# Optimization experiments

Hardware: AMD Instinct MI355X
Metric: run time of the kernel (lower is better)

## Reference

```python
import jax, jax.numpy as jnp
import numpy as np

EPS = 1e-5
B, CIN, COUT, H, W = 32, 512, 512, 56, 56
K = 4            # kernel_num
A = 32           # attention_channel = max(int(512*0.0625), 16)


def setup_inputs() -> dict:
    key = jax.random.key(0)
    ks = jax.random.split(key, 16)
    s = lambda fan: 1.0 / np.sqrt(fan)
    return {
        "x": jax.random.normal(ks[0], (B, CIN, H, W), jnp.float32),
        # attention trunk: global-avgpool -> fc -> bn -> relu
        "fc_w": jax.random.normal(ks[1], (A, CIN), jnp.float32) * s(CIN),
        "abn_g": jnp.ones((A,), jnp.float32),
        "abn_b": jnp.zeros((A,), jnp.float32),
        "abn_m": jax.random.normal(ks[2], (A,), jnp.float32) * 0.1,
        "abn_v": jax.random.uniform(ks[3], (A,), jnp.float32, 0.5, 1.5),
        # channel / filter / kernel attention heads
        "ch_w": jax.random.normal(ks[4], (CIN, A), jnp.float32) * s(A),
        "ch_b": jnp.zeros((CIN,), jnp.float32),
        "fl_w": jax.random.normal(ks[5], (COUT, A), jnp.float32) * s(A),
        "fl_b": jnp.zeros((COUT,), jnp.float32),
        "kn_w": jax.random.normal(ks[6], (K, A), jnp.float32) * s(A),
        "kn_b": jnp.zeros((K,), jnp.float32),
        # base 1x1 conv weight bank [kernel_num, out, in] (1x1 spatial squeezed)
        "weight": jax.random.normal(ks[7], (K, COUT, CIN), jnp.float32) * s(CIN),
        # output BatchNorm2d (eval mode: running stats)
        "bn_g": jnp.ones((COUT,), jnp.float32),
        "bn_b": jnp.zeros((COUT,), jnp.float32),
        "bn_m": jax.random.normal(ks[8], (COUT,), jnp.float32) * 0.1,
        "bn_v": jax.random.uniform(ks[9], (COUT,), jnp.float32, 0.5, 1.5),
    }


def reference(x, fc_w, abn_g, abn_b, abn_m, abn_v,
              ch_w, ch_b, fl_w, fl_b, kn_w, kn_b,
              weight, bn_g, bn_b, bn_m, bn_v):
    # ---- omni-dimensional attention (kernel_size=1 => spatial attn skipped) ----
    pooled = jnp.mean(x, axis=(2, 3))                       # [B, Cin]
    h = pooled @ fc_w.T                                     # [B, A]
    h = (h - abn_m) * (abn_g / jnp.sqrt(abn_v + EPS)) + abn_b
    h = jax.nn.relu(h)
    ch_att = jax.nn.sigmoid(h @ ch_w.T + ch_b)              # [B, Cin]
    fl_att = jax.nn.sigmoid(h @ fl_w.T + fl_b)              # [B, Cout]
    kn_att = jax.nn.softmax(h @ kn_w.T + kn_b, axis=1)      # [B, K] (temperature=1)
    # ---- per-sample aggregated 1x1 kernel + grouped(batch) pointwise conv ----
    agg_w = jnp.einsum('bk,koc->boc', kn_att, weight)       # [B, Cout, Cin]
    xm = x * ch_att[:, :, None, None]                       # channel attention
    y = jnp.einsum('bchw,boc->bohw', xm, agg_w)             # batched 1x1 conv
    y = y * fl_att[:, :, None, None]                        # filter attention
    # ---- BatchNorm2d (inference) ----
    inv = bn_g / jnp.sqrt(bn_v + EPS)
    y = (y - bn_m[None, :, None, None]) * inv[None, :, None, None] + bn_b[None, :, None, None]
    return y
```

## Files before the change

### kernel.cpp

```cpp
#include <hip/hip_runtime.h>
#include <math.h>

#define BATCH 32
#define CIN   512
#define COUT  512
#define HW    3136
#define KNUM  4
#define ADIM  32
#define EPS   1e-5f

static constexpr size_t XT_OFF    = 0;
static constexpr size_t WF_OFF    = 102760448;
static constexpr size_t PART_OFF  = 119537664;
static constexpr size_t CH_OFF    = 122748928;
static constexpr size_t FLINV_OFF = 122814464;
static constexpr size_t KN_OFF    = 122880000;

typedef __attribute__((ext_vector_type(8))) short short8;
typedef __attribute__((ext_vector_type(4))) float float4v;

typedef const unsigned int __attribute__((address_space(1)))* gas_ptr;
typedef unsigned int __attribute__((address_space(3)))* lds_ptr;

__device__ __forceinline__ unsigned short f2bf(float f) {
  unsigned int u = __float_as_uint(f);
  u += 0x7FFFu + ((u >> 16) & 1u);
  return (unsigned short)(u >> 16);
}

__global__ __launch_bounds__(256) void transpose_pool(
    const float* __restrict__ x, unsigned short* __restrict__ xT,
    float* __restrict__ part) {
  __shared__ unsigned short T[64 * 68];
  const int pb    = blockIdx.x * 64;
  const int cbase = blockIdx.y * 256;
  const int b     = blockIdx.z;
  const int t  = threadIdx.x;
  const int mp = t & 15;
  const int mc = t >> 4;
  const int p0 = pb + mp * 4;
  const int pr = t >> 2, cp = t & 3;

  #pragma unroll
  for (int sub = 0; sub < 4; ++sub) {
    const int cb = cbase + sub * 64;
    const int c0 = cb + mc * 4;
    const float* xp = x + (size_t)(b * CIN + c0) * HW + p0;
    float a[4][4];
    #pragma unroll
    for (int r = 0; r < 4; ++r) {
      float4 v = *(const float4*)(xp + (size_t)r * HW);
      a[r][0] = v.x; a[r][1] = v.y; a[r][2] = v.z; a[r][3] = v.w;
      float s = v.x + v.y + v.z + v.w;
      #pragma unroll
      for (int off = 8; off > 0; off >>= 1) s += __shfl_down(s, off, 16);
      if (mp == 0)
        part[((size_t)b * 49 + blockIdx.x) * 512 + c0 + r] = s;
    }
    #pragma unroll
    for (int j = 0; j < 4; ++j) {
      ushort4 w;
      w.x = f2bf(a[0][j]); w.y = f2bf(a[1][j]);
      w.z = f2bf(a[2][j]); w.w = f2bf(a[3][j]);
      *(ushort4*)&T[(mp * 4 + j) * 68 + mc * 4] = w;
    }
    __syncthreads();
    const int base = pr * 68 + cp * 16;
    uint2 r0 = *(uint2*)&T[base + 0];
    uint2 r1 = *(uint2*)&T[base + 4];
    uint2 r2 = *(uint2*)&T[base + 8];
    uint2 r3 = *(uint2*)&T[base + 12];
    unsigned short* dst = xT + (size_t)(b * HW + pb + pr) * CIN + cb + cp * 16;
    *(uint4*)(dst)     = make_uint4(r0.x, r0.y, r1.x, r1.y);
    *(uint4*)(dst + 8) = make_uint4(r2.x, r2.y, r3.x, r3.y);
    __syncthreads();
  }
}

__global__ __launch_bounds__(256) void attn_all(
    const float* __restrict__ part, const float* __restrict__ fc_w,
    const float* __restrict__ abn_g, const float* __restrict__ abn_b,
    const float* __restrict__ abn_m, const float* __restrict__ abn_v,
    const float* __restrict__ kn_w, const float* __restrict__ kn_b,
    const float* __restrict__ ch_w, const float* __restrict__ ch_b,
    const float* __restrict__ fl_w, const float* __restrict__ fl_b,
    const float* __restrict__ bn_g, const float* __restrict__ bn_v,
    float* __restrict__ ch_out, float* __restrict__ flinv_out,
    float* __restrict__ kn_out) {
  __shared__ float pooledS[CIN];
  __shared__ float hs[ADIM];
  const int b = blockIdx.x, t = threadIdx.x;
  #pragma unroll
  for (int idx = t; idx < CIN; idx += 256) {
    float s = 0.f;
    for (int j = 0; j < 49; ++j) s += part[((size_t)b * 49 + j) * 512 + idx];
    pooledS[idx] = s;
  }
  __syncthreads();
  {
    const int a = t >> 3, pz = t & 7;
    const float* fr = fc_w + a * CIN + pz * 64;
    const float* pp = pooledS + pz * 64;
    float s = 0.f;
    #pragma unroll 8
    for (int c = 0; c < 64; ++c) s += pp[c] * fr[c];
    #pragma unroll
    for (int off = 4; off > 0; off >>= 1) s += __shfl_down(s, off, 8);
    if (pz == 0) {
      s *= (1.0f / (float)HW);
      float vv = (s - abn_m[a]) * (abn_g[a] * rsqrtf(abn_v[a] + EPS)) + abn_b[a];
      hs[a] = fmaxf(vv, 0.f);
    }
  }
  __syncthreads();
  if (t == 0) {
    float lg[KNUM]; float mx = -1e30f;
    for (int k = 0; k < KNUM; ++k) {
      float acc = kn_b[k];
      for (int aa = 0; aa < ADIM; ++aa) acc += hs[aa] * kn_w[k * ADIM + aa];
      lg[k] = acc; mx = fmaxf(mx, acc);
    }
    float ssum = 0.f;
    for (int k = 0; k < KNUM; ++k) { lg[k] = expf(lg[k] - mx); ssum += lg[k]; }
    for (int k = 0; k < KNUM; ++k) kn_out[b * KNUM + k] = lg[k] / ssum;
  }
  #pragma unroll
  for (int c = t; c < CIN; c += 256) {
    const float* wr = ch_w + c * ADIM;
    float acc = ch_b[c];
    #pragma unroll
    for (int aa = 0; aa < ADIM; ++aa) acc += hs[aa] * wr[aa];
    ch_out[b * CIN + c] = 1.f / (1.f + expf(-acc));
  }
  #pragma unroll
  for (int o = t; o < COUT; o += 256) {
    const float* wr = fl_w + o * ADIM;
    float acc = fl_b[o];
    #pragma unroll
    for (int aa = 0; aa < ADIM; ++aa) acc += hs[aa] * wr[aa];
    float sig = 1.f / (1.f + expf(-acc));
    flinv_out[b * COUT + o] = sig * (bn_g[o] * rsqrtf(bn_v[o] + EPS));
  }
}

__global__ __launch_bounds__(256) void build_wf(
    const float* __restrict__ weight, const float* __restrict__ kn,
    const float* __restrict__ ch, const float* __restrict__ flinv,
    unsigned short* __restrict__ Wf) {
  const int och = blockIdx.x, b = blockIdx.y, t = threadIdx.x;
  const int o0 = och * 16;
  const float k0 = kn[b * KNUM + 0], k1 = kn[b * KNUM + 1];
  const float k2 = kn[b * KNUM + 2], k3 = kn[b * KNUM + 3];
  #pragma unroll
  for (int i = 0; i < 8; ++i) {
    int cell = i * 1024 + t * 4;
    int ol = cell >> 9, c = cell & 511;
    int o = o0 + ol;
    float fi = flinv[b * COUT + o];
    const float* wp = weight + (size_t)o * CIN + c;
    float4 w0 = *(const float4*)(wp);
    float4 w1 = *(const float4*)(wp + 1 * CIN * COUT);
    float4 w2 = *(const float4*)(wp + 2 * CIN * COUT);
    float4 w3 = *(const float4*)(wp + 3 * CIN * COUT);
    float4 cv = *(const float4*)(ch + b * CIN + c);
    ushort4 r;
    r.x = f2bf((k0 * w0.x + k1 * w1.x + k2 * w2.x + k3 * w3.x) * cv.x * fi);
    r.y = f2bf((k0 * w0.y + k1 * w1.y + k2 * w2.y + k3 * w3.y) * cv.y * fi);
    r.z = f2bf((k0 * w0.z + k1 * w1.z + k2 * w2.z + k3 * w3.z) * cv.z * fi);
    r.w = f2bf((k0 * w0.w + k1 * w1.w + k2 * w2.w + k3 * w3.w) * cv.w * fi);
    *(ushort4*)(Wf + (size_t)(b * COUT + o) * CIN + c) = r;
  }
}

__global__ __launch_bounds__(256, 4) void gemm_kernel(
    const unsigned short* __restrict__ xT, const unsigned short* __restrict__ Wf,
    const float* __restrict__ bn_g, const float* __restrict__ bn_b,
    const float* __restrict__ bn_m, const float* __restrict__ bn_v,
    float* __restrict__ y) {
  __shared__ unsigned short lA[128 * 64];
  __shared__ unsigned short lB[128 * 64];
  const int ot = blockIdx.x, pt = blockIdx.y, b = blockIdx.z;
  const int o0 = ot * 128, p0 = pt * 128;
  const int t = threadIdx.x;
  const int wave = t >> 6, lane = t & 63;
  const int wm = wave & 1, wn = wave >> 1;

  const int srow = lane >> 3;
  const int sgrp = lane & 7;
  const int scol = ((sgrp ^ srow) * 8);

  const unsigned short* Ab = Wf + (size_t)b * COUT * CIN;
  const unsigned short* Bb = xT + (size_t)b * HW * CIN;
  const unsigned short* aSrc[4];
  const unsigned short* bSrc[4];
  #pragma unroll
  for (int q = 0; q < 4; ++q) {
    const int ar = o0 + wave * 32 + q * 8 + srow;
    aSrc[q] = Ab + (size_t)ar * CIN + scol;
    int br = p0 + wave * 32 + q * 8 + srow;
    if (br > HW - 1) br = HW - 1;
    bSrc[q] = Bb + (size_t)br * CIN + scol;
  }

  float4v acc[4][4];
  #pragma unroll
  for (int i = 0; i < 4; ++i)
    #pragma unroll
    for (int j = 0; j < 4; ++j)
      #pragma unroll
      for (int r = 0; r < 4; ++r) acc[i][j][r] = 0.f;

  const int arow = lane & 15;
  const int kgrp = lane >> 4;
  const int slot0 = ((0 + kgrp) ^ (arow & 7)) * 8;
  const int slot1 = ((4 + kgrp) ^ (arow & 7)) * 8;

  for (int kt = 0; kt < CIN / 64; ++kt) {
    const int c0 = kt * 64;
    __syncthreads();
    #pragma unroll
    for (int q = 0; q < 4; ++q) {
      __builtin_amdgcn_global_load_lds((gas_ptr)(const void*)(aSrc[q] + c0),
          (lds_ptr)(void*)&lA[(wave * 32 + q * 8) * 64], 16, 0, 0);
      __builtin_amdgcn_global_load_lds((gas_ptr)(const void*)(bSrc[q] + c0),
          (lds_ptr)(void*)&lB[(wave * 32 + q * 8) * 64], 16, 0, 0);
    }
    __syncthreads();

    #pragma unroll
    for (int ks = 0; ks < 2; ++ks) {
      const int sl = ks ? slot1 : slot0;
      short8 af[4], bfr[4];
      #pragma unroll
      for (int i = 0; i < 4; ++i)
        af[i] = *(const short8*)&lA[(wm * 64 + i * 16 + arow) * 64 + sl];
      #pragma unroll
      for (int j = 0; j < 4; ++j)
        bfr[j] = *(const short8*)&lB[(wn * 64 + j * 16 + arow) * 64 + sl];
      #pragma unroll
      for (int i = 0; i < 4; ++i)
        #pragma unroll
        for (int j = 0; j < 4; ++j)
          acc[i][j] = __builtin_amdgcn_mfma_f32_16x16x32_bf16(af[i], bfr[j], acc[i][j], 0, 0, 0);
    }
  }

  const int rowq = (lane >> 4) * 4;
  const int coln = lane & 15;
  #pragma unroll
  for (int i = 0; i < 4; ++i) {
    const int obase = o0 + wm * 64 + i * 16 + rowq;
    float bet[4];
    #pragma unroll
    for (int r = 0; r < 4; ++r) {
      const int o = obase + r;
      const float inv = bn_g[o] * rsqrtf(bn_v[o] + EPS);
      bet[r] = bn_b[o] - bn_m[o] * inv;
    }
    #pragma unroll
    for (int j = 0; j < 4; ++j) {
      const int p = p0 + wn * 64 + j * 16 + coln;
      if (p < HW) {
        #pragma unroll
        for (int r = 0; r < 4; ++r)
          y[(size_t)(b * COUT + obase + r) * HW + p] = acc[i][j][r] + bet[r];
      }
    }
  }
}

extern "C" void kernel_launch(void* const* d_in, const int* in_sizes, int n_in,
                              void* d_out, int out_size, void* d_ws, size_t ws_size,
                              hipStream_t stream) {
  (void)in_sizes; (void)n_in; (void)out_size; (void)ws_size;
  const float* x     = (const float*)d_in[0];
  const float* fc_w  = (const float*)d_in[1];
  const float* abn_g = (const float*)d_in[2];
  const float* abn_b = (const float*)d_in[3];
  const float* abn_m = (const float*)d_in[4];
  const float* abn_v = (const float*)d_in[5];
  const float* ch_w  = (const float*)d_in[6];
  const float* ch_b  = (const float*)d_in[7];
  const float* fl_w  = (const float*)d_in[8];
  const float* fl_b  = (const float*)d_in[9];
  const float* kn_w  = (const float*)d_in[10];
  const float* kn_b  = (const float*)d_in[11];
  const float* weight= (const float*)d_in[12];
  const float* bn_g  = (const float*)d_in[13];
  const float* bn_b  = (const float*)d_in[14];
  const float* bn_m  = (const float*)d_in[15];
  const float* bn_v  = (const float*)d_in[16];
  float* out = (float*)d_out;

  char* ws = (char*)d_ws;
  unsigned short* xT = (unsigned short*)(ws + XT_OFF);
  unsigned short* Wf = (unsigned short*)(ws + WF_OFF);
  float* part  = (float*)(ws + PART_OFF);
  float* ch    = (float*)(ws + CH_OFF);
  float* flinv = (float*)(ws + FLINV_OFF);
  float* kn    = (float*)(ws + KN_OFF);

  transpose_pool<<<dim3(49, 2, BATCH), 256, 0, stream>>>(x, xT, part);
  attn_all<<<BATCH, 256, 0, stream>>>(part, fc_w, abn_g, abn_b, abn_m, abn_v,
                                      kn_w, kn_b, ch_w, ch_b, fl_w, fl_b,
                                      bn_g, bn_v, ch, flinv, kn);
  build_wf<<<dim3(32, BATCH), 256, 0, stream>>>(weight, kn, ch, flinv, Wf);
  gemm_kernel<<<dim3(4, 25, BATCH), 256, 0, stream>>>(xT, Wf, bn_g, bn_b, bn_m, bn_v, out);
}
```

Before: 496.7 us.

## Restructure transpose-pool kernel with XOR-swizzled LDS tile and single sync

Each transpose_pool block now covers a 64-pixel by 128-channel tile instead of looping over four 64-channel sub-tiles with two barriers each. Each thread packs two channels as bf16 pairs into an XOR-swizzled shared tile, so a single barrier is enough and the write-out is full 16-byte rows with fewer bank conflicts. The pooled partial sums are reduced with shuffles after all loads have been issued, and the grid doubles along the channel dimension. The aim is more parallelism and memory-level overlap in this bandwidth-bound prologue, at the cost of a larger shared-memory tile.

```diff
diff --git a/kernel.cpp b/kernel.cpp
--- a/kernel.cpp
+++ b/kernel.cpp
@@ -31,49 +31,55 @@
 __global__ __launch_bounds__(256) void transpose_pool(
     const float* __restrict__ x, unsigned short* __restrict__ xT,
     float* __restrict__ part) {
-  __shared__ unsigned short T[64 * 68];
-  const int pb    = blockIdx.x * 64;
-  const int cbase = blockIdx.y * 256;
-  const int b     = blockIdx.z;
+  __shared__ unsigned short T[64 * 128];
+  const int pb = blockIdx.x * 64;
+  const int cb = blockIdx.y * 128;
+  const int b  = blockIdx.z;
   const int t  = threadIdx.x;
-  const int mp = t & 15;
-  const int mc = t >> 4;
-  const int p0 = pb + mp * 4;
-  const int pr = t >> 2, cp = t & 3;
-
-  #pragma unroll
-  for (int sub = 0; sub < 4; ++sub) {
-    const int cb = cbase + sub * 64;
-    const int c0 = cb + mc * 4;
-    const float* xp = x + (size_t)(b * CIN + c0) * HW + p0;
-    float a[4][4];
-    #pragma unroll
-    for (int r = 0; r < 4; ++r) {
-      float4 v = *(const float4*)(xp + (size_t)r * HW);
-      a[r][0] = v.x; a[r][1] = v.y; a[r][2] = v.z; a[r][3] = v.w;
-      float s = v.x + v.y + v.z + v.w;
-      #pragma unroll
-      for (int off = 8; off > 0; off >>= 1) s += __shfl_down(s, off, 16);
-      if (mp == 0)
-        part[((size_t)b * 49 + blockIdx.x) * 512 + c0 + r] = s;
-    }
+  const int pq = t & 15;
+  const int ch = t >> 4;
+
+  float s[4][2];
+  #pragma unroll
+  for (int it = 0; it < 4; ++it) {
+    const int cp = it * 16 + ch;
+    const int c  = cb + cp * 2;
+    const float* xp = x + (size_t)(b * CIN + c) * HW + pb + pq * 4;
+    float4 v0 = *(const float4*)(xp);
+    float4 v1 = *(const float4*)(xp + HW);
+    s[it][0] = v0.x + v0.y + v0.z + v0.w;
+    s[it][1] = v1.x + v1.y + v1.z + v1.w;
+    const int dbase = (((cp >> 2) ^ pq) & 15) * 4 + (cp & 3);
+    const float* f0 = (const float*)&v0;
+    const float* f1 = (const float*)&v1;
     #pragma unroll
     for (int j = 0; j < 4; ++j) {
-      ushort4 w;
-      w.x = f2bf(a[0][j]); w.y = f2bf(a[1][j]);
-      w.z = f2bf(a[2][j]); w.w = f2bf(a[3][j]);
-      *(ushort4*)&T[(mp * 4 + j) * 68 + mc * 4] = w;
-    }
-    __syncthreads();
-    const int base = pr * 68 + cp * 16;
-    uint2 r0 = *(uint2*)&T[base + 0];
-    uint2 r1 = *(uint2*)&T[base + 4];
-    uint2 r2 = *(uint2*)&T[base + 8];
-    uint2 r3 = *(uint2*)&T[base + 12];
-    unsigned short* dst = xT + (size_t)(b * HW + pb + pr) * CIN + cb + cp * 16;
-    *(uint4*)(dst)     = make_uint4(r0.x, r0.y, r1.x, r1.y);
-    *(uint4*)(dst + 8) = make_uint4(r2.x, r2.y, r3.x, r3.y);
-    __syncthreads();
+      const int p = pq * 4 + j;
+      unsigned int w = (unsigned int)f2bf(f0[j]) |
+                       ((unsigned int)f2bf(f1[j]) << 16);
+      *(unsigned int*)&T[p * 128 + dbase * 2] = w;
+    }
+  }
+  #pragma unroll
+  for (int it = 0; it < 4; ++it) {
+    #pragma unroll
+    for (int e = 0; e < 2; ++e) {
+      float v = s[it][e];
+      #pragma unroll
+      for (int off = 8; off > 0; off >>= 1) v += __shfl_down(v, off, 16);
+      if (pq == 0)
+        part[((size_t)b * 49 + blockIdx.x) * 512 + cb + (it * 16 + ch) * 2 + e] = v;
+    }
+  }
+  __syncthreads();
+  const int cg = t & 15;
+  const int rb = t >> 4;
+  #pragma unroll
+  for (int itr = 0; itr < 4; ++itr) {
+    const int p = rb + itr * 16;
+    const int key = (p >> 2) & 15;
+    uint4 r = *(const uint4*)&T[p * 128 + ((cg ^ key) & 15) * 8];
+    *(uint4*)(xT + (size_t)(b * HW + pb + p) * CIN + cb + cg * 8) = r;
   }
 }
 
@@ -300,7 +306,7 @@
   float* flinv = (float*)(ws + FLINV_OFF);
   float* kn    = (float*)(ws + KN_OFF);
 
-  transpose_pool<<<dim3(49, 2, BATCH), 256, 0, stream>>>(x, xT, part);
+  transpose_pool<<<dim3(49, 4, BATCH), 256, 0, stream>>>(x, xT, part);
   attn_all<<<BATCH, 256, 0, stream>>>(part, fc_w, abn_g, abn_b, abn_m, abn_v,
                                       kn_w, kn_b, ch_w, ch_b, fl_w, fl_b,
                                       bn_g, bn_v, ch, flinv, kn);
```

After: 491.4 us. No clear change (-1.1%).
